# Kernel optimization log

Measured on AMD Instinct MI355X. Metric: run time of the kernel, lower is better.

Reference implementation:

```python
import jax, jax.numpy as jnp
import numpy as np

H, L, N = 512, 2048, 64  # channels, seq len, SSM state size


def _make_dplr_hippo(n):
    # make_HiPPO / make_NPLR_HiPPO / make_DPLR_HiPPO from the source
    p0 = np.sqrt(1.0 + 2.0 * np.arange(n))
    A = p0[:, None] * p0[None, :]
    A = np.tril(A) - np.diag(np.arange(n))
    nhippo = -A
    P = np.sqrt(np.arange(n) + 0.5)
    B = np.sqrt(2.0 * np.arange(n) + 1.0)
    S = nhippo + P[:, None] * P[None, :]
    S_diag = np.diagonal(S)
    Lam_re = np.mean(S_diag) * np.ones_like(S_diag)
    Lam_im, V = jnp.linalg.eigh(jnp.asarray(S, jnp.complex64) * (-1j))
    Pc = V.conj().T @ jnp.asarray(P, jnp.complex64)
    Bc = V.conj().T @ jnp.asarray(B, jnp.complex64)
    return (jnp.asarray(Lam_re, jnp.float32), jnp.asarray(Lam_im, jnp.float32),
            Pc, Bc)


def setup_inputs() -> dict:
    key = jax.random.key(0)
    k_u, k_c, k_s = jax.random.split(key, 3)
    Lre, Lim, Pc, Bc = _make_dplr_hippo(N)
    tile = lambda v: jnp.tile(v[None, :], (H, 1)).astype(jnp.float32)  # (H,N)
    return {
        "u": jax.random.normal(k_u, (L, H), dtype=jnp.float32),
        "x0_re": jnp.zeros((N, H), jnp.float32),
        "x0_im": jnp.zeros((N, H), jnp.float32),
        "Lambda_re": tile(Lre),
        "Lambda_im": tile(Lim),
        "P_re": tile(Pc.real), "P_im": tile(Pc.imag),
        "B_re": tile(Bc.real), "B_im": tile(Bc.imag),
        "C": jax.random.normal(k_c, (H, N, 2), jnp.float32) * (0.5 ** 0.5),
        "D": jnp.ones((H, 1), jnp.float32),
        "log_step": jax.random.uniform(k_s, (H, 1), jnp.float32,
                                       minval=np.log(1e-3), maxval=np.log(1e-1)),
    }


def _discretize(Lam, P, B, Ct, step):
    # discrete_DPLR with Q = P (as in setup); per-channel, vmapped over H.
    n = Lam.shape[0]
    I = jnp.eye(n, dtype=jnp.complex64)
    A = jnp.diag(Lam) - P[:, None] * P.conj()[None, :]
    A0 = (2.0 / step) * I + A
    Dd = jnp.diag(1.0 / (2.0 / step - Lam))
    Qc = P.conj()[None, :]            # (1,N)
    P2 = P[:, None]                   # (N,1)
    A1 = Dd - (Dd @ P2) * (1.0 / (1.0 + Qc @ Dd @ P2)) * (Qc @ Dd)
    Ab = A1 @ A0                      # (N,N)
    Bb = 2.0 * (A1 @ B[:, None])[:, 0]
    AbL = jnp.linalg.matrix_power(Ab, L)
    Cb = (Ct[None, :] @ jnp.linalg.inv(I - AbL).conj()).conj()[0]
    return Ab, Bb, Cb


def _forward(u, x0_re, x0_im, Lambda_re, Lambda_im, P_re, P_im,
             B_re, B_im, C, D, log_step):
    Lam = jnp.clip(Lambda_re, None, -0.0001) + 1j * Lambda_im  # (H,N)
    Pc = P_re + 1j * P_im
    Bc = B_re + 1j * B_im
    Cc = C[..., 0] + 1j * C[..., 1]
    step = jnp.exp(log_step)[:, 0]                              # (H,)
    Ab, Bb, Cb = jax.vmap(_discretize)(Lam, Pc, Bc, Cc, step)   # (H,N,N),(H,N),(H,N)

    x0 = jnp.transpose(x0_re + 1j * x0_im)                      # (H,N) complex

    def body(x, u_t):  # x: (H,N) complex, u_t: (H,)
        x = jnp.einsum('hnm,hm->hn', Ab, x) + Bb * u_t[:, None]
        y = jnp.einsum('hn,hn->h', Cb, x)
        return x, y.real

    _, ys = jax.lax.scan(body, x0, u)                           # ys: (L,H)
    return ys + u * D[:, 0][None, :]                            # (L,H) float32


def reference(u, x0_re, x0_im, Lambda_re, Lambda_im, P_re, P_im,
              B_re, B_im, C, D, log_step):
    return _forward(u, x0_re, x0_im, Lambda_re, Lambda_im, P_re, P_im,
                    B_re, B_im, C, D, log_step)
```

## Files before the change

### kernel.cpp

```cpp
#include <hip/hip_runtime.h>

#define HH 512
#define LL 2048
#define NN 64
#define TT 64
#define CC 32
#define NLDA 68
#define SP 72

typedef __attribute__((ext_vector_type(8))) short bf16x8_t;
typedef __attribute__((ext_vector_type(4))) float floatx4;

__device__ __forceinline__ float2 cmul(float2 a, float2 b) {
    return make_float2(a.x * b.x - a.y * b.y, a.x * b.y + a.y * b.x);
}
__device__ __forceinline__ float2 crecip(float2 a) {
    float id = 1.0f / (a.x * a.x + a.y * a.y);
    return make_float2(a.x * id, -a.y * id);
}
template <int CTRL>
__device__ __forceinline__ float dpp_mov(float x) {
    return __int_as_float(__builtin_amdgcn_update_dpp(
        0, __float_as_int(x), CTRL, 0xf, 0xf, true));
}
__device__ __forceinline__ float wave_sum_bcast(float x) {
    x += dpp_mov<0x111>(x);
    x += dpp_mov<0x112>(x);
    x += dpp_mov<0x114>(x);
    x += dpp_mov<0x118>(x);
    x += dpp_mov<0x142>(x);
    x += dpp_mov<0x143>(x);
    return __int_as_float(__builtin_amdgcn_readlane(__float_as_int(x), 63));
}
__device__ __forceinline__ float rlane(float x, int i) {
    return __int_as_float(__builtin_amdgcn_readlane(__float_as_int(x), i));
}
__device__ __forceinline__ unsigned short f2bf(float f) {
    unsigned int u = __float_as_uint(f);
    u += 0x7FFFu + ((u >> 16) & 1u);
    return (unsigned short)(u >> 16);
}
__device__ __forceinline__ float bf2f(unsigned short s) {
    return __uint_as_float(((unsigned int)s) << 16);
}

__device__ __forceinline__ void closed_form(
    int h, int n,
    const float* __restrict__ Lre, const float* __restrict__ Lim,
    const float* __restrict__ Pre, const float* __restrict__ Pim,
    const float* __restrict__ Bre, const float* __restrict__ Bim,
    const float* __restrict__ logstep,
    float2& da, float2& DPv, float2& tv, float2& bb) {
    float step = expf(logstep[h]);
    float as = 2.0f / step;
    float lr = fminf(Lre[h * NN + n], -1e-4f);
    float li = Lim[h * NN + n];
    float2 a = make_float2(as + lr, li);
    float2 Dn = crecip(make_float2(as - lr, -li));
    float2 P = make_float2(Pre[h * NN + n], Pim[h * NN + n]);
    float2 Bv = make_float2(Bre[h * NN + n], Bim[h * NN + n]);
    float2 cP = make_float2(P.x, -P.y);
    float p2 = P.x * P.x + P.y * P.y;
    float2 rt = cmul(cmul(cP, Dn), Bv);
    float2 e = make_float2(wave_sum_bcast(Dn.x * p2), wave_sum_bcast(Dn.y * p2));
    float2 rv = make_float2(wave_sum_bcast(rt.x), wave_sum_bcast(rt.y));
    float2 cc = crecip(make_float2(1.0f + e.x, e.y));
    da = cmul(Dn, a);
    DPv = cmul(Dn, P);
    float2 tmp = cmul(cc, make_float2(da.x - e.x, da.y - e.y));
    tv = cmul(cP, make_float2(1.0f + tmp.x, tmp.y));
    float2 crv = cmul(cc, rv);
    float2 cd = cmul(crv, DPv);
    float2 db = cmul(Dn, Bv);
    bb = make_float2(2.0f * (db.x - cd.x), 2.0f * (db.y - cd.y));
}

__device__ __forceinline__ void pack_tiles(
    unsigned short* mRh, unsigned short* mRl,
    unsigned short* mIh, unsigned short* mIl,
    unsigned short* mTRh, unsigned short* mTRl,
    unsigned short* mTIh, unsigned short* mTIl,
    int w, int lm, int q, const float Cr[4][4], const float Ci[4][4]) {
    #pragma unroll
    for (int nt = 0; nt < 4; ++nt) {
        const int c = nt * 16 + lm;
        unsigned short hr[4], lr_[4], hi_[4], li_[4];
        #pragma unroll
        for (int reg = 0; reg < 4; ++reg) {
            const float xr = Cr[nt][reg], xi = Ci[nt][reg];
            hr[reg] = f2bf(xr); lr_[reg] = f2bf(xr - bf2f(hr[reg]));
            hi_[reg] = f2bf(xi); li_[reg] = f2bf(xi - bf2f(hi_[reg]));
            const int r = 16 * w + 4 * q + reg;
            mRh[r * SP + c] = hr[reg]; mRl[r * SP + c] = lr_[reg];
            mIh[r * SP + c] = hi_[reg]; mIl[r * SP + c] = li_[reg];
        }
        const int tb = c * SP + 16 * w + 4 * q;
        *(ushort4*)&mTRh[tb] = make_ushort4(hr[0], hr[1], hr[2], hr[3]);
        *(ushort4*)&mTRl[tb] = make_ushort4(lr_[0], lr_[1], lr_[2], lr_[3]);
        *(ushort4*)&mTIh[tb] = make_ushort4(hi_[0], hi_[1], hi_[2], hi_[3]);
        *(ushort4*)&mTIl[tb] = make_ushort4(li_[0], li_[1], li_[2], li_[3]);
    }
}

extern "C" __global__ void __launch_bounds__(256, 2)
k_fusedA(const float* __restrict__ Lre, const float* __restrict__ Lim,
         const float* __restrict__ Pre, const float* __restrict__ Pim,
         const float* __restrict__ Bre, const float* __restrict__ Bim,
         const float* __restrict__ Cmat, const float* __restrict__ logstep,
         float2* __restrict__ wM, float2* __restrict__ wCb) {
    extern __shared__ __align__(16) char smem[];
    const int tid = threadIdx.x;
    const int h = blockIdx.x;

    unsigned short* mRh  = (unsigned short*)smem;
    unsigned short* mRl  = mRh + 64 * SP;
    unsigned short* mIh  = mRl + 64 * SP;
    unsigned short* mIl  = mIh + 64 * SP;
    unsigned short* mTRh = mIl + 64 * SP;
    unsigned short* mTRl = mTRh + 64 * SP;
    unsigned short* mTIh = mTRl + 64 * SP;
    unsigned short* mTIl = mTIh + 64 * SP;
    float* Nr = (float*)smem;
    float* Ni = Nr + 64 * NLDA;
    float2* sda  = (float2*)(smem + 73728);
    float2* sDP  = sda + NN;
    float2* st   = sDP + NN;
    float2* sBb  = st + NN;
    float2* srhs = sBb + NN;
    float2* sx   = srhs + NN;
    float2* pp   = sx + NN;

    const int w = tid >> 6;
    const int lane = tid & 63;
    const int lm = lane & 15, q = lane >> 4;

    if (tid < NN) {
        float2 da, DPv, tv, bb;
        closed_form(h, tid, Lre, Lim, Pre, Pim, Bre, Bim, logstep,
                    da, DPv, tv, bb);
        sda[tid] = da; sDP[tid] = DPv; st[tid] = tv; sBb[tid] = bb;
        srhs[tid] = make_float2(Cmat[h * NN * 2 + tid * 2],
                                -Cmat[h * NN * 2 + tid * 2 + 1]);
    }
    __syncthreads();

    {
        float Cr[4][4], Ci[4][4];
        #pragma unroll
        for (int nt = 0; nt < 4; ++nt) {
            const int c = nt * 16 + lm;
            const float2 tc = st[c];
            #pragma unroll
            for (int reg = 0; reg < 4; ++reg) {
                const int r = 16 * w + 4 * q + reg;
                const float2 dp = sDP[r];
                float vr = -(dp.x * tc.x - dp.y * tc.y);
                float vi = -(dp.x * tc.y + dp.y * tc.x);
                if (r == c) { vr += sda[r].x; vi += sda[r].y; }
                Cr[nt][reg] = vr; Ci[nt][reg] = vi;
            }
        }
        pack_tiles(mRh, mRl, mIh, mIl, mTRh, mTRl, mTIh, mTIl,
                   w, lm, q, Cr, Ci);
    }
    __syncthreads();

    const int arow = (16 * w + lm) * SP + q * 8;
    for (int it = 0; it < 11; ++it) {
        floatx4 z4 = {0.f, 0.f, 0.f, 0.f};
        floatx4 aP[4] = {z4, z4, z4, z4};
        floatx4 aQ[4] = {z4, z4, z4, z4};
        floatx4 aC[4] = {z4, z4, z4, z4};
        for (int k2 = 0; k2 < 2; ++k2) {
            const int ao = arow + k2 * 32;
            const bf16x8_t ARh = *(const bf16x8_t*)&mRh[ao];
            const bf16x8_t ARl = *(const bf16x8_t*)&mRl[ao];
            const bf16x8_t AIh = *(const bf16x8_t*)&mIh[ao];
            const bf16x8_t AIl = *(const bf16x8_t*)&mIl[ao];
            bf16x8_t BRh[4], BRl[4], BIh[4], BIl[4];
            #pragma unroll
            for (int nt = 0; nt < 4; ++nt) {
                const int bo = (nt * 16 + lm) * SP + k2 * 32 + q * 8;
                BRh[nt] = *(const bf16x8_t*)&mTRh[bo];
                BRl[nt] = *(const bf16x8_t*)&mTRl[bo];
                BIh[nt] = *(const bf16x8_t*)&mTIh[bo];
                BIl[nt] = *(const bf16x8_t*)&mTIl[bo];
            }
            #pragma unroll
            for (int nt = 0; nt < 4; ++nt) {
                aP[nt] = __builtin_amdgcn_mfma_f32_16x16x32_bf16(ARh, BRh[nt], aP[nt], 0, 0, 0);
                aP[nt] = __builtin_amdgcn_mfma_f32_16x16x32_bf16(ARh, BRl[nt], aP[nt], 0, 0, 0);
                aP[nt] = __builtin_amdgcn_mfma_f32_16x16x32_bf16(ARl, BRh[nt], aP[nt], 0, 0, 0);
                aQ[nt] = __builtin_amdgcn_mfma_f32_16x16x32_bf16(AIh, BIh[nt], aQ[nt], 0, 0, 0);
                aQ[nt] = __builtin_amdgcn_mfma_f32_16x16x32_bf16(AIh, BIl[nt], aQ[nt], 0, 0, 0);
                aQ[nt] = __builtin_amdgcn_mfma_f32_16x16x32_bf16(AIl, BIh[nt], aQ[nt], 0, 0, 0);
                aC[nt] = __builtin_amdgcn_mfma_f32_16x16x32_bf16(ARh, BIh[nt], aC[nt], 0, 0, 0);
                aC[nt] = __builtin_amdgcn_mfma_f32_16x16x32_bf16(ARh, BIl[nt], aC[nt], 0, 0, 0);
                aC[nt] = __builtin_amdgcn_mfma_f32_16x16x32_bf16(ARl, BIh[nt], aC[nt], 0, 0, 0);
                aC[nt] = __builtin_amdgcn_mfma_f32_16x16x32_bf16(AIh, BRh[nt], aC[nt], 0, 0, 0);
                aC[nt] = __builtin_amdgcn_mfma_f32_16x16x32_bf16(AIh, BRl[nt], aC[nt], 0, 0, 0);
                aC[nt] = __builtin_amdgcn_mfma_f32_16x16x32_bf16(AIl, BRh[nt], aC[nt], 0, 0, 0);
            }
        }
        __syncthreads();
        if (it < 10) {
            float Cr[4][4], Ci[4][4];
            #pragma unroll
            for (int nt = 0; nt < 4; ++nt)
                #pragma unroll
                for (int reg = 0; reg < 4; ++reg) {
                    Cr[nt][reg] = aP[nt][reg] - aQ[nt][reg];
                    Ci[nt][reg] = aC[nt][reg];
                }
            pack_tiles(mRh, mRl, mIh, mIl, mTRh, mTRl, mTIh, mTIl,
                       w, lm, q, Cr, Ci);
            __syncthreads();
            if (it == 5) {
                for (int idx = tid; idx < NN * NN; idx += 256) {
                    const int c = idx >> 6, k = idx & 63;
                    wM[h * NN * NN + idx] = make_float2(
                        bf2f(mTRh[c * SP + k]) + bf2f(mTRl[c * SP + k]),
                        bf2f(mTIh[c * SP + k]) + bf2f(mTIl[c * SP + k]));
                }
            }
        } else {
            #pragma unroll
            for (int nt = 0; nt < 4; ++nt) {
                const int c = nt * 16 + lm;
                #pragma unroll
                for (int reg = 0; reg < 4; ++reg) {
                    const int r = 16 * w + 4 * q + reg;
                    Nr[r * NLDA + c] = aP[nt][reg] - aQ[nt][reg];
                    Ni[r * NLDA + c] = aC[nt][reg];
                }
            }
            __syncthreads();
        }
    }

    if (tid < NN) sx[tid] = srhs[tid];
    __syncthreads();
    for (int itn = 0; itn < 16; ++itn) {
        const int i = tid & 63, qq = tid >> 6;
        float pr = 0.0f, pi = 0.0f;
        #pragma unroll 4
        for (int jj = 0; jj < 16; ++jj) {
            const int j = qq * 16 + jj;
            const float nr = Nr[j * NLDA + i], ni = Ni[j * NLDA + i];
            const float2 xj = sx[j];
            pr += nr * xj.x - ni * xj.y;
            pi += nr * xj.y + ni * xj.x;
        }
        pp[qq * 64 + i] = make_float2(pr, pi);
        __syncthreads();
        if (tid < NN) {
            const float2 a0 = pp[tid], a1 = pp[64 + tid];
            const float2 a2 = pp[128 + tid], a3 = pp[192 + tid];
            sx[tid] = make_float2(
                srhs[tid].x + a0.x + a1.x + a2.x + a3.x,
                srhs[tid].y + a0.y + a1.y + a2.y + a3.y);
        }
        __syncthreads();
    }
    if (tid < NN) wCb[h * NN + tid] = sx[tid];
}

extern "C" __global__ void __launch_bounds__(256, 2)
k_fusedB(const float* __restrict__ Lre, const float* __restrict__ Lim,
         const float* __restrict__ Pre, const float* __restrict__ Pim,
         const float* __restrict__ Bre, const float* __restrict__ Bim,
         const float* __restrict__ logstep,
         const float* __restrict__ u, const float* __restrict__ Dvec,
         const float* __restrict__ x0_re, const float* __restrict__ x0_im,
         const float2* __restrict__ wM, const float2* __restrict__ wCb,
         float* __restrict__ out) {
    extern __shared__ __align__(16) char smem[];
    unsigned short* sVr  = (unsigned short*)smem;
    unsigned short* sVi  = (unsigned short*)(smem + 9216);
    unsigned short* sXrh = (unsigned short*)(smem + 18432);
    unsigned short* sXrl = (unsigned short*)(smem + 23040);
    unsigned short* sXih = (unsigned short*)(smem + 27648);
    unsigned short* sXil = (unsigned short*)(smem + 32256);
    float*          su   = (float*)(smem + 36864);
    float*          sK   = (float*)(smem + 45056);
    float*          y0   = (float*)(smem + 45312);
    float2*         sP   = (float2*)(smem + 53632);

    const int h = blockIdx.x;
    const int tid = threadIdx.x;
    const int wv = tid >> 6, lane = tid & 63;
    const int lm = lane & 15, q = lane >> 4;

    float Mr[NN], Mi[NN];
    float x0r = 0.0f, x0i = 0.0f;

    if (wv == 0) {
        float2 da, DP, tt, Bb;
        closed_form(h, lane, Lre, Lim, Pre, Pim, Bre, Bim, logstep,
                    da, DP, tt, Bb);
        const float2 Cb = wCb[h * NN + lane];
        float Gr = Bb.x, Gi = Bb.y;
        float vr = Cb.x, vi = Cb.y;
        for (int m = 0; m < TT; ++m) {
            float ch[5];
            ch[0] = Cb.x * Gr - Cb.y * Gi;
            ch[1] = tt.x * Gr - tt.y * Gi;
            ch[2] = tt.x * Gi + tt.y * Gr;
            ch[3] = vr * DP.x - vi * DP.y;
            ch[4] = vr * DP.y + vi * DP.x;
            #pragma unroll
            for (int c = 0; c < 5; ++c) ch[c] += dpp_mov<0x111>(ch[c]);
            #pragma unroll
            for (int c = 0; c < 5; ++c) ch[c] += dpp_mov<0x112>(ch[c]);
            #pragma unroll
            for (int c = 0; c < 5; ++c) ch[c] += dpp_mov<0x114>(ch[c]);
            #pragma unroll
            for (int c = 0; c < 5; ++c) ch[c] += dpp_mov<0x118>(ch[c]);
            #pragma unroll
            for (int c = 0; c < 5; ++c) ch[c] += dpp_mov<0x142>(ch[c]);
            #pragma unroll
            for (int c = 0; c < 5; ++c) ch[c] += dpp_mov<0x143>(ch[c]);
            const float S0 = rlane(ch[0], 63);
            const float S1 = rlane(ch[1], 63);
            const float S2 = rlane(ch[2], 63);
            const float S3 = rlane(ch[3], 63);
            const float S4 = rlane(ch[4], 63);
            if (lane == 0) sK[m] = S0;
            float nGr = da.x * Gr - da.y * Gi - (DP.x * S1 - DP.y * S2);
            float nGi = da.x * Gi + da.y * Gr - (DP.x * S2 + DP.y * S1);
            Gr = nGr; Gi = nGi;
            float nvr = da.x * vr - da.y * vi - (S3 * tt.x - S4 * tt.y);
            float nvi = da.x * vi + da.y * vr - (S3 * tt.y + S4 * tt.x);
            vr = nvr; vi = nvi;
            sVr[m * SP + lane] = f2bf(vr);
            sVi[m * SP + lane] = f2bf(-vi);
        }
    } else if (wv == 1) {
        const float2* __restrict__ wMh = wM + h * NN * NN;
        #pragma unroll
        for (int j = 0; j < NN; ++j) {
            const float2 v = wMh[j * NN + lane];
            Mr[j] = v.x; Mi[j] = v.y;
        }
        x0r = x0_re[lane * HH + h];
        x0i = x0_im[lane * HH + h];
    } else {
        const int par = wv - 2;
        for (int k = lane; k < 1024; k += 64) {
            const int cc = ((k >> 6) << 1) | par;
            const int s = k & 63;
            su[cc * 64 + s] = u[(cc * 64 + s) * HH + h];
        }
        float2 da, DP, tt, Bb;
        closed_form(h, lane, Lre, Lim, Pre, Pim, Bre, Bim, logstep,
                    da, DP, tt, Bb);
        float Gr = Bb.x, Gi = Bb.y;
        float ar[16] = {}, ai[16] = {};
        for (int m = 0; m < TT; ++m) {
            #pragma unroll
            for (int ci = 0; ci < 16; ++ci) {
                const int cc = (ci << 1) | par;
                const float uv = su[cc * 64 + (63 - m)];
                ar[ci] = fmaf(Gr, uv, ar[ci]);
                ai[ci] = fmaf(Gi, uv, ai[ci]);
            }
            float c1 = tt.x * Gr - tt.y * Gi;
            float c2 = tt.x * Gi + tt.y * Gr;
            c1 += dpp_mov<0x111>(c1); c2 += dpp_mov<0x111>(c2);
            c1 += dpp_mov<0x112>(c1); c2 += dpp_mov<0x112>(c2);
            c1 += dpp_mov<0x114>(c1); c2 += dpp_mov<0x114>(c2);
            c1 += dpp_mov<0x118>(c1); c2 += dpp_mov<0x118>(c2);
            c1 += dpp_mov<0x142>(c1); c2 += dpp_mov<0x142>(c2);
            c1 += dpp_mov<0x143>(c1); c2 += dpp_mov<0x143>(c2);
            const float S1 = rlane(c1, 63);
            const float S2 = rlane(c2, 63);
            float nGr = da.x * Gr - da.y * Gi - (DP.x * S1 - DP.y * S2);
            float nGi = da.x * Gi + da.y * Gr - (DP.x * S2 + DP.y * S1);
            Gr = nGr; Gi = nGi;
        }
        #pragma unroll
        for (int ci = 0; ci < 16; ++ci) {
            const int cc = (ci << 1) | par;
            sP[cc * 64 + lane] = make_float2(ar[ci], ai[ci]);
        }
    }
    __syncthreads();

    const float Dh = Dvec[h];
    if (wv == 1) {
        float xr = x0r, xi = x0i;
        {
            const unsigned short hr = f2bf(xr), hi_ = f2bf(xi);
            sXrh[lane] = hr;  sXrl[lane] = f2bf(xr - bf2f(hr));
            sXih[lane] = hi_; sXil[lane] = f2bf(xi - bf2f(hi_));
        }
        for (int c = 1; c < CC; ++c) {
            const float2 pe = sP[(c - 1) * 64 + lane];
            float ar[4] = {0.f, 0.f, 0.f, 0.f};
            float ai[4] = {0.f, 0.f, 0.f, 0.f};
            #pragma unroll
            for (int j = 0; j < NN; ++j) {
                const float xjr = rlane(xr, j);
                const float xji = rlane(xi, j);
                ar[j & 3] = fmaf(Mr[j], xjr, ar[j & 3]);
                ar[j & 3] = fmaf(-Mi[j], xji, ar[j & 3]);
                ai[j & 3] = fmaf(Mr[j], xji, ai[j & 3]);
                ai[j & 3] = fmaf(Mi[j], xjr, ai[j & 3]);
            }
            xr = ((ar[0] + ar[1]) + (ar[2] + ar[3])) + pe.x;
            xi = ((ai[0] + ai[1]) + (ai[2] + ai[3])) + pe.y;
            const unsigned short hr = f2bf(xr), hi_ = f2bf(xi);
            sXrh[c * SP + lane] = hr;  sXrl[c * SP + lane] = f2bf(xr - bf2f(hr));
            sXih[c * SP + lane] = hi_; sXil[c * SP + lane] = f2bf(xi - bf2f(hi_));
        }
    } else {
        const int c0 = (wv == 0) ? 0 : (wv == 2 ? 11 : 22);
        const int c1 = (wv == 0) ? 11 : (wv == 2 ? 22 : 32);
        for (int c = c0; c < c1; ++c) {
            float acc = 0.0f;
            for (int s = 0; s < TT; ++s) {
                const int d = lane - s;
                const float kv = (d >= 0) ? sK[d < 0 ? 0 : d] : 0.0f;
                acc = fmaf(kv, su[c * 64 + s], acc);
            }
            y0[c * 65 + lane] = acc + Dh * su[c * 64 + lane];
        }
    }
    __syncthreads();

    floatx4 z4 = {0.f, 0.f, 0.f, 0.f};
    floatx4 acc2[2] = {z4, z4};
    #pragma unroll
    for (int k2 = 0; k2 < 2; ++k2) {
        const int ak = (16 * wv + lm) * SP + k2 * 32 + q * 8;
        const bf16x8_t aVr = *(const bf16x8_t*)&sVr[ak];
        const bf16x8_t aVi = *(const bf16x8_t*)&sVi[ak];
        #pragma unroll
        for (int nt = 0; nt < 2; ++nt) {
            const int bk = (nt * 16 + lm) * SP + k2 * 32 + q * 8;
            const bf16x8_t bRh = *(const bf16x8_t*)&sXrh[bk];
            const bf16x8_t bRl = *(const bf16x8_t*)&sXrl[bk];
            const bf16x8_t bIh = *(const bf16x8_t*)&sXih[bk];
            const bf16x8_t bIl = *(const bf16x8_t*)&sXil[bk];
            acc2[nt] = __builtin_amdgcn_mfma_f32_16x16x32_bf16(aVr, bRh, acc2[nt], 0, 0, 0);
            acc2[nt] = __builtin_amdgcn_mfma_f32_16x16x32_bf16(aVr, bRl, acc2[nt], 0, 0, 0);
            acc2[nt] = __builtin_amdgcn_mfma_f32_16x16x32_bf16(aVi, bIh, acc2[nt], 0, 0, 0);
            acc2[nt] = __builtin_amdgcn_mfma_f32_16x16x32_bf16(aVi, bIl, acc2[nt], 0, 0, 0);
        }
    }
    #pragma unroll
    for (int nt = 0; nt < 2; ++nt) {
        #pragma unroll
        for (int reg = 0; reg < 4; ++reg) {
            const int c = nt * 16 + lm;
            const int t = 16 * wv + 4 * q + reg;
            out[(c * TT + t) * HH + h] = acc2[nt][reg] + y0[c * 65 + t];
        }
    }
}

extern "C" void kernel_launch(void* const* d_in, const int* in_sizes, int n_in,
                              void* d_out, int out_size, void* d_ws, size_t ws_size,
                              hipStream_t stream) {
    const float* u    = (const float*)d_in[0];
    const float* x0re = (const float*)d_in[1];
    const float* x0im = (const float*)d_in[2];
    const float* Lre  = (const float*)d_in[3];
    const float* Lim  = (const float*)d_in[4];
    const float* Pre  = (const float*)d_in[5];
    const float* Pim  = (const float*)d_in[6];
    const float* Bre  = (const float*)d_in[7];
    const float* Bim  = (const float*)d_in[8];
    const float* C    = (const float*)d_in[9];
    const float* Dv   = (const float*)d_in[10];
    const float* lst  = (const float*)d_in[11];

    float2* wM  = (float2*)d_ws;
    float2* wCb = wM + HH * NN * NN;
    float* out = (float*)d_out;

    hipLaunchKernelGGL(k_fusedA, dim3(HH), dim3(256), 78848, stream,
                       Lre, Lim, Pre, Pim, Bre, Bim, C, lst,
                       wM, wCb);
    hipLaunchKernelGGL(k_fusedB, dim3(HH), dim3(256), 70016, stream,
                       Lre, Lim, Pre, Pim, Bre, Bim, lst, u, Dv,
                       x0re, x0im, wM, wCb, out);
}
```

Baseline: 205.4 us.

## Fuse discretization and scan kernels into one per-channel kernel

New measurement: 263.6 us. 1.28x slower.

```diff
diff --git a/kernel.cpp b/kernel.cpp
--- a/kernel.cpp
+++ b/kernel.cpp
@@ -103,11 +103,13 @@
 }
 
 extern "C" __global__ void __launch_bounds__(256, 2)
-k_fusedA(const float* __restrict__ Lre, const float* __restrict__ Lim,
-         const float* __restrict__ Pre, const float* __restrict__ Pim,
-         const float* __restrict__ Bre, const float* __restrict__ Bim,
-         const float* __restrict__ Cmat, const float* __restrict__ logstep,
-         float2* __restrict__ wM, float2* __restrict__ wCb) {
+k_fused(const float* __restrict__ Lre, const float* __restrict__ Lim,
+        const float* __restrict__ Pre, const float* __restrict__ Pim,
+        const float* __restrict__ Bre, const float* __restrict__ Bim,
+        const float* __restrict__ Cmat, const float* __restrict__ logstep,
+        const float* __restrict__ u, const float* __restrict__ Dvec,
+        const float* __restrict__ x0_re, const float* __restrict__ x0_im,
+        float* __restrict__ out) {
     extern __shared__ __align__(16) char smem[];
     const int tid = threadIdx.x;
     const int h = blockIdx.x;
@@ -129,10 +131,22 @@
     float2* srhs = sBb + NN;
     float2* sx   = srhs + NN;
     float2* pp   = sx + NN;
+    unsigned short* sVr  = (unsigned short*)smem;
+    unsigned short* sVi  = (unsigned short*)(smem + 9216);
+    unsigned short* sXrh = (unsigned short*)(smem + 18432);
+    unsigned short* sXrl = (unsigned short*)(smem + 23040);
+    unsigned short* sXih = (unsigned short*)(smem + 27648);
+    unsigned short* sXil = (unsigned short*)(smem + 32256);
+    float*          su   = (float*)(smem + 36864);
+    float*          sK   = (float*)(smem + 45056);
+    float*          y0   = (float*)(smem + 45312);
+    float2*         sP   = (float2*)(smem + 53632);
 
     const int w = tid >> 6;
     const int lane = tid & 63;
     const int lm = lane & 15, q = lane >> 4;
+
+    float Mr[NN] = {}, Mi[NN] = {};
 
     if (tid < NN) {
         float2 da, DPv, tv, bb;
@@ -215,12 +229,11 @@
             pack_tiles(mRh, mRl, mIh, mIl, mTRh, mTRl, mTIh, mTIl,
                        w, lm, q, Cr, Ci);
             __syncthreads();
-            if (it == 5) {
-                for (int idx = tid; idx < NN * NN; idx += 256) {
-                    const int c = idx >> 6, k = idx & 63;
-                    wM[h * NN * NN + idx] = make_float2(
-                        bf2f(mTRh[c * SP + k]) + bf2f(mTRl[c * SP + k]),
-                        bf2f(mTIh[c * SP + k]) + bf2f(mTIl[c * SP + k]));
+            if (it == 5 && w == 1) {
+                #pragma unroll
+                for (int j = 0; j < NN; ++j) {
+                    Mr[j] = bf2f(mRh[lane * SP + j]) + bf2f(mRl[lane * SP + j]);
+                    Mi[j] = bf2f(mIh[lane * SP + j]) + bf2f(mIl[lane * SP + j]);
                 }
             }
         } else {
@@ -262,43 +275,14 @@
         }
         __syncthreads();
     }
-    if (tid < NN) wCb[h * NN + tid] = sx[tid];
-}
-
-extern "C" __global__ void __launch_bounds__(256, 2)
-k_fusedB(const float* __restrict__ Lre, const float* __restrict__ Lim,
-         const float* __restrict__ Pre, const float* __restrict__ Pim,
-         const float* __restrict__ Bre, const float* __restrict__ Bim,
-         const float* __restrict__ logstep,
-         const float* __restrict__ u, const float* __restrict__ Dvec,
-         const float* __restrict__ x0_re, const float* __restrict__ x0_im,
-         const float2* __restrict__ wM, const float2* __restrict__ wCb,
-         float* __restrict__ out) {
-    extern __shared__ __align__(16) char smem[];
-    unsigned short* sVr  = (unsigned short*)smem;
-    unsigned short* sVi  = (unsigned short*)(smem + 9216);
-    unsigned short* sXrh = (unsigned short*)(smem + 18432);
-    unsigned short* sXrl = (unsigned short*)(smem + 23040);
-    unsigned short* sXih = (unsigned short*)(smem + 27648);
-    unsigned short* sXil = (unsigned short*)(smem + 32256);
-    float*          su   = (float*)(smem + 36864);
-    float*          sK   = (float*)(smem + 45056);
-    float*          y0   = (float*)(smem + 45312);
-    float2*         sP   = (float2*)(smem + 53632);
-
-    const int h = blockIdx.x;
-    const int tid = threadIdx.x;
-    const int wv = tid >> 6, lane = tid & 63;
-    const int lm = lane & 15, q = lane >> 4;
-
-    float Mr[NN], Mi[NN];
+
+    const int wv = w;
     float x0r = 0.0f, x0i = 0.0f;
 
     if (wv == 0) {
-        float2 da, DP, tt, Bb;
-        closed_form(h, lane, Lre, Lim, Pre, Pim, Bre, Bim, logstep,
-                    da, DP, tt, Bb);
-        const float2 Cb = wCb[h * NN + lane];
+        const float2 da = sda[lane], DP = sDP[lane], tt = st[lane];
+        const float2 Bb = sBb[lane];
+        const float2 Cb = sx[lane];
         float Gr = Bb.x, Gi = Bb.y;
         float vr = Cb.x, vi = Cb.y;
         for (int m = 0; m < TT; ++m) {
@@ -336,12 +320,6 @@
             sVi[m * SP + lane] = f2bf(-vi);
         }
     } else if (wv == 1) {
-        const float2* __restrict__ wMh = wM + h * NN * NN;
-        #pragma unroll
-        for (int j = 0; j < NN; ++j) {
-            const float2 v = wMh[j * NN + lane];
-            Mr[j] = v.x; Mi[j] = v.y;
-        }
         x0r = x0_re[lane * HH + h];
         x0i = x0_im[lane * HH + h];
     } else {
@@ -351,9 +329,8 @@
             const int s = k & 63;
             su[cc * 64 + s] = u[(cc * 64 + s) * HH + h];
         }
-        float2 da, DP, tt, Bb;
-        closed_form(h, lane, Lre, Lim, Pre, Pim, Bre, Bim, logstep,
-                    da, DP, tt, Bb);
+        const float2 da = sda[lane], DP = sDP[lane], tt = st[lane];
+        const float2 Bb = sBb[lane];
         float Gr = Bb.x, Gi = Bb.y;
         float ar[16] = {}, ai[16] = {};
         for (int m = 0; m < TT; ++m) {
@@ -428,8 +405,8 @@
     }
     __syncthreads();
 
-    floatx4 z4 = {0.f, 0.f, 0.f, 0.f};
-    floatx4 acc2[2] = {z4, z4};
+    floatx4 z4b = {0.f, 0.f, 0.f, 0.f};
+    floatx4 acc2[2] = {z4b, z4b};
     #pragma unroll
     for (int k2 = 0; k2 < 2; ++k2) {
         const int ak = (16 * wv + lm) * SP + k2 * 32 + q * 8;
@@ -474,15 +451,9 @@
     const float* C    = (const float*)d_in[9];
     const float* Dv   = (const float*)d_in[10];
     const float* lst  = (const float*)d_in[11];
-
-    float2* wM  = (float2*)d_ws;
-    float2* wCb = wM + HH * NN * NN;
     float* out = (float*)d_out;
 
-    hipLaunchKernelGGL(k_fusedA, dim3(HH), dim3(256), 78848, stream,
-                       Lre, Lim, Pre, Pim, Bre, Bim, C, lst,
-                       wM, wCb);
-    hipLaunchKernelGGL(k_fusedB, dim3(HH), dim3(256), 70016, stream,
-                       Lre, Lim, Pre, Pim, Bre, Bim, lst, u, Dv,
-                       x0re, x0im, wM, wCb, out);
-}
+    hipLaunchKernelGGL(k_fused, dim3(HH), dim3(256), 78848, stream,
+                       Lre, Lim, Pre, Pim, Bre, Bim, C, lst, u, Dv,
+                       x0re, x0im, out);
+}
```
